# Kernel optimization log

Hardware: AMD Instinct MI355X
Metric: run time of the kernel (lower is better)

The kernel has to match this reference:

```python
import jax, jax.numpy as jnp
import numpy as np
from jax import lax

D, B, C, H, HD, FF, NC = 6, 32, 384, 6, 64, 1536, 10
IMG, P = 224, 16
N = (IMG // P) ** 2 + 1  # 197 tokens incl cls
SCALE = HD ** -0.5
EPS = 1e-6


def ln(x, w, b):
    m = jnp.mean(x, axis=-1, keepdims=True)
    v = jnp.var(x, axis=-1, keepdims=True)
    return (x - m) * lax.rsqrt(v + EPS) * w + b


def setup_inputs() -> dict:
    key = jax.random.key(0)
    ks = iter(jax.random.split(key, 40))
    rn = lambda shape, s=0.02: jax.random.normal(next(ks), shape, jnp.float32) * s
    inp = {
        'x': jax.random.normal(next(ks), (B, 3, IMG, IMG), jnp.float32),
        'y': jax.random.randint(next(ks), (B,), 0, NC),
        'patch_w': rn((C, 3, P, P)),
        'patch_b': rn((C,)),
        'cls_token': rn((1, 1, C)),
        'pos_embed': rn((1, N, C)),
        'n1_w': jnp.ones((D, C)), 'n1_b': jnp.zeros((D, C)),
        'qkv_w': rn((D, 3 * C, C)), 'qkv_b': rn((D, 3 * C)),
        'proj_w': rn((D, C, C)), 'proj_b': rn((D, C)),
        'mask_attn': jnp.ones((D, NC, H, HD)) + rn((D, NC, H, HD), 0.01),
        'mask_proj': jnp.ones((D, NC, C, C)) + rn((D, NC, C, C), 0.01),
        'n2_w': jnp.ones((D, C)), 'n2_b': jnp.zeros((D, C)),
        'fc1_w': rn((D, FF, C)), 'fc1_b': rn((D, FF)),
        'fc2_w': rn((D, C, FF)), 'fc2_b': rn((D, C)),
        'mask_fc1': jnp.ones((D, NC, FF, C)) + rn((D, NC, FF, C), 0.01),
        'mask_fc2': jnp.ones((D, NC, C, FF)) + rn((D, NC, C, FF), 0.01),
        'norm_w': jnp.ones((C,)), 'norm_b': jnp.zeros((C,)),
        'head_w': rn((NC, C)), 'head_b': jnp.zeros((NC,)),
    }
    return inp


def reference(x, y, patch_w, patch_b, cls_token, pos_embed, n1_w, n1_b, qkv_w,
              qkv_b, proj_w, proj_b, mask_attn, mask_proj, n2_w, n2_b,
              fc1_w, fc1_b, fc2_w, fc2_b, mask_fc1, mask_fc2,
              norm_w, norm_b, head_w, head_b):
    # patch embed: conv P x P stride P -> (B, C, 14, 14) -> (B, 196, C)
    h = lax.conv_general_dilated(x, patch_w, (P, P), 'VALID',
                                 dimension_numbers=('NCHW', 'OIHW', 'NCHW'))
    h = h.reshape(B, C, -1).transpose(0, 2, 1) + patch_b
    h = jnp.concatenate([jnp.broadcast_to(cls_token, (B, 1, C)), h], axis=1)
    h = h + pos_embed

    def block(xc, p):
        (w1n, b1n, qw, qb, pw, pb, ma, mp, w2n, b2n,
         f1w, f1b, f2w, f2b, mf1, mf2) = p
        t = ln(xc, w1n, b1n)
        qkv = (t @ qw.T + qb).reshape(B, N, 3, H, HD).transpose(2, 0, 3, 1, 4)
        q, k, v = qkv[0], qkv[1], qkv[2]  # (B,H,N,HD)
        a = jax.nn.softmax((q * SCALE) @ k.transpose(0, 1, 3, 2), axis=-1)
        o = a @ v  # (B,H,N,HD)
        o = o * ma[y][:, :, None, :]  # per-class head/dim mask
        o = o.transpose(0, 2, 1, 3).reshape(B, N, C)
        Wp = pw[None] * mp[y]  # (B,C,C) per-sample masked proj
        attn_out = jnp.einsum('bni,boi->bno', o, Wp) + pb
        xc = xc + attn_out
        t = ln(xc, w2n, b2n)
        W1 = f1w[None] * mf1[y]  # (B,FF,C)
        t = jnp.einsum('bni,boi->bno', t, W1) + f1b
        t = jax.nn.gelu(t, approximate=False)
        W2 = f2w[None] * mf2[y]  # (B,C,FF)
        t = jnp.einsum('bni,boi->bno', t, W2) + f2b
        return xc + t, None

    xs = (n1_w, n1_b, qkv_w, qkv_b, proj_w, proj_b, mask_attn, mask_proj,
          n2_w, n2_b, fc1_w, fc1_b, fc2_w, fc2_b, mask_fc1, mask_fc2)
    h, _ = lax.scan(block, h, xs)
    h = ln(h, norm_w, norm_b)
    cls = h[:, 0]  # (B, C)
    return cls @ head_w.T + head_b
```

## Files before the change

### kernel.cpp

```cpp
#include <hip/hip_runtime.h>
#include <hip/hip_bf16.h>
#include <math.h>

#define Dn 6
#define Bn 32
#define Cn 384
#define Hn 6
#define HDn 64
#define FFn 1536
#define NCn 10
#define IMGn 224
#define Nn 197
#define NPATCH 196
#define RP 256
#define SCALEf 0.125f
#define EPSf 1e-6f

typedef unsigned short u16;
typedef __attribute__((ext_vector_type(8))) short short8;
typedef __attribute__((ext_vector_type(4))) float f32x4;

__device__ __forceinline__ u16 f2bf(float f) {
    unsigned u = __float_as_uint(f);
    return (u16)((u + 0x7FFFu + ((u >> 16) & 1u)) >> 16);
}

__device__ __forceinline__ void gload16(const void* g, void* l) {
    __builtin_amdgcn_global_load_lds((const __attribute__((address_space(1))) void*)g,
                                     (__attribute__((address_space(3))) void*)l, 16, 0, 0);
}

__global__ __launch_bounds__(256) void cvtbf_kernel(const float* __restrict__ in,
                                                    u16* __restrict__ out) {
    long off = ((long)blockIdx.x * 256 + threadIdx.x) * 8;
    float4 v0 = *(const float4*)(in + off);
    float4 v1 = *(const float4*)(in + off + 4);
    short8 p;
    p[0] = f2bf(v0.x); p[1] = f2bf(v0.y); p[2] = f2bf(v0.z); p[3] = f2bf(v0.w);
    p[4] = f2bf(v1.x); p[5] = f2bf(v1.y); p[6] = f2bf(v1.z); p[7] = f2bf(v1.w);
    *(short8*)(out + off) = p;
}

__global__ __launch_bounds__(256) void maskmul_kernel(const float* __restrict__ W,
                                                      const float* __restrict__ mask,
                                                      u16* __restrict__ out, int NK) {
    int c = blockIdx.y;
    long off = ((long)blockIdx.x * 256 + threadIdx.x) * 8;
    long coff = (long)c * NK + off;
    float4 w0 = *(const float4*)(W + off);
    float4 w1 = *(const float4*)(W + off + 4);
    float4 m0 = *(const float4*)(mask + coff);
    float4 m1 = *(const float4*)(mask + coff + 4);
    short8 p;
    p[0] = f2bf(w0.x * m0.x); p[1] = f2bf(w0.y * m0.y);
    p[2] = f2bf(w0.z * m0.z); p[3] = f2bf(w0.w * m0.w);
    p[4] = f2bf(w1.x * m1.x); p[5] = f2bf(w1.y * m1.y);
    p[6] = f2bf(w1.z * m1.z); p[7] = f2bf(w1.w * m1.w);
    *(short8*)(out + coff) = p;
}

__global__ __launch_bounds__(256) void im2col_kernel(const float* __restrict__ x,
                                                     u16* __restrict__ col) {
    long idx = (long)blockIdx.x * 256 + threadIdx.x;
    int k = (int)(idx % 768);
    long row = idx / 768;
    int b = (int)(row / NPATCH), p = (int)(row % NPATCH);
    int i = k / 256, r = k % 256, ph = r / 16, pw = r % 16;
    int py = p / 14, px = p % 14;
    col[idx] = f2bf(x[(((long)b * 3 + i) * IMGn + py * 16 + ph) * IMGn + px * 16 + pw]);
}

__global__ __launch_bounds__(256) void assemble_kernel(const float* __restrict__ tmp,
                                                       const float* __restrict__ cls_token,
                                                       const float* __restrict__ pos,
                                                       float* __restrict__ x) {
    long idx = (long)blockIdx.x * 256 + threadIdx.x;
    const long total = (long)Bn * Nn * Cn;
    if (idx >= total) return;
    int c = (int)(idx % Cn);
    long rem = idx / Cn;
    int n = (int)(rem % Nn);
    int b = (int)(rem / Nn);
    float v;
    if (n == 0) v = cls_token[c];
    else v = tmp[((long)b * NPATCH + (n - 1)) * Cn + c];
    x[((long)b * RP + n) * Cn + c] = v + pos[n * Cn + c];
}

__global__ __launch_bounds__(64) void ln_kernel(const float* __restrict__ x,
                                                const float* __restrict__ w,
                                                const float* __restrict__ b,
                                                u16* __restrict__ out) {
    long blk = blockIdx.x;
    int bb = (int)(blk / Nn), n = (int)(blk % Nn);
    long row = (long)bb * RP + n;
    int lane = threadIdx.x;
    const float* xr = x + row * Cn;
    float v[6];
    float s = 0.f, ss = 0.f;
#pragma unroll
    for (int j = 0; j < 6; ++j) {
        v[j] = xr[lane + 64 * j];
        s += v[j];
        ss += v[j] * v[j];
    }
#pragma unroll
    for (int off = 32; off >= 1; off >>= 1) {
        s += __shfl_xor(s, off);
        ss += __shfl_xor(ss, off);
    }
    float m = s * (1.0f / Cn);
    float var = ss * (1.0f / Cn) - m * m;
    float rstd = rsqrtf(var + EPSf);
#pragma unroll
    for (int j = 0; j < 6; ++j) {
        int c = lane + 64 * j;
        out[row * Cn + c] = f2bf((v[j] - m) * rstd * w[c] + b[c]);
    }
}

template <int EPI, int KSPLIT>
__global__ __launch_bounds__(256) void gemm_bf16(
    const u16* __restrict__ A, long strideA,
    const u16* __restrict__ Wb, long wClassStride,
    const int* __restrict__ y,
    const float* __restrict__ bias,
    void* __restrict__ OutV, long strideO,
    int Nout, int Ktot, int NTILES) {
    const int bz = blockIdx.z;
    const int nt = blockIdx.y % NTILES;
    const int ks = blockIdx.y / NTILES;
    const int K2 = Ktot / KSPLIT;
    const int kbeg = ks * K2;
    A += (long)bz * strideA;
    const u16* Wp = Wb + (y ? (long)y[bz] * wClassStride : 0);

    __shared__ alignas(16) u16 Ab[4096];
    __shared__ alignas(16) u16 Bb[4096];

    const int tid = threadIdx.x;
    const int lane = tid & 63;
    const int w = tid >> 6;
    const int wr = w >> 1, wc = w & 1;
    const int m0 = blockIdx.x * 128;
    const int n0 = nt * 128;

    const int srow = 2 * w * 16 + (lane & 15);
    const int gk = (lane >> 4) * 8;

    f32x4 acc[4][4];
#pragma unroll
    for (int i = 0; i < 4; ++i)
#pragma unroll
        for (int j = 0; j < 4; ++j) acc[i][j] = (f32x4){0.f, 0.f, 0.f, 0.f};

    for (int k0 = kbeg; k0 < kbeg + K2; k0 += 32) {
        const u16* a0 = A + (long)(m0 + srow) * Ktot + k0 + gk;
        const u16* b0 = Wp + (long)(n0 + srow) * Ktot + k0 + gk;
        gload16(a0, Ab + 2 * w * 512);
        gload16(a0 + 16 * (long)Ktot, Ab + (2 * w + 1) * 512);
        gload16(b0, Bb + 2 * w * 512);
        gload16(b0 + 16 * (long)Ktot, Bb + (2 * w + 1) * 512);
        __syncthreads();
        short8 af[4], bfr[4];
#pragma unroll
        for (int i = 0; i < 4; ++i)
            af[i] = *(const short8*)(Ab + (wr * 4 + i) * 512 + lane * 8);
#pragma unroll
        for (int j = 0; j < 4; ++j)
            bfr[j] = *(const short8*)(Bb + (wc * 4 + j) * 512 + lane * 8);
#pragma unroll
        for (int i = 0; i < 4; ++i)
#pragma unroll
            for (int j = 0; j < 4; ++j)
                acc[i][j] = __builtin_amdgcn_mfma_f32_16x16x32_bf16(af[i], bfr[j], acc[i][j], 0, 0, 0);
        __syncthreads();
    }

    const int lr = lane >> 4;
    const int lc = lane & 15;
#pragma unroll
    for (int i = 0; i < 4; ++i) {
#pragma unroll
        for (int j = 0; j < 4; ++j) {
            int colg = n0 + (wc * 4 + j) * 16 + lc;
            float bv = (bias && ks == 0) ? bias[colg] : 0.f;
#pragma unroll
            for (int r = 0; r < 4; ++r) {
                int m = m0 + (wr * 4 + i) * 16 + lr * 4 + r;
                float v = acc[i][j][r] + bv;
                long oi = (long)m * Nout + colg;
                if (EPI == 0) {
                    ((u16*)OutV + (long)bz * strideO)[oi] = f2bf(v);
                } else if (EPI == 1) {
                    v = 0.5f * v * (1.0f + erff(v * 0.70710678118654752440f));
                    ((u16*)OutV + (long)bz * strideO)[oi] = f2bf(v);
                } else if (EPI == 2) {
                    float* Out = (float*)OutV + (long)bz * strideO;
                    if (KSPLIT > 1) atomicAdd(Out + oi, v);
                    else Out[oi] += v;
                } else {
                    ((float*)OutV + (long)bz * strideO)[oi] = v;
                }
            }
        }
    }
}

__global__ __launch_bounds__(256) void attn_fused(const u16* __restrict__ qkv,
                                                  const float* __restrict__ ma,
                                                  const int* __restrict__ y,
                                                  u16* __restrict__ O) {
    const int it = blockIdx.x;
    const int bh = blockIdx.y;
    const int h = bh % Hn, b = bh / Hn;
    const int i0 = it * 64;
    const int tid = threadIdx.x, lane = tid & 63, w = tid >> 6;
    const int lg = lane >> 4, lc = lane & 15;

    __shared__ alignas(16) u16 SH[31744];
    u16* Qb = SH;
    u16* Kb = SH + 4096;
    u16* Vb = SH;
    u16* Pb = SH + 17408;

    const u16* qkv_b = qkv + (long)b * RP * (3 * Cn);
    const int r15 = lane & 15;
    const int oct = lane >> 4;

#pragma unroll
    for (int si = 0; si < 2; ++si) {
        int s = w * 2 + si;
        int r = (s >> 1) * 16 + r15;
        int g = (s & 1) * 4 + oct;
        const u16* src = qkv_b + (long)(i0 + r) * (3 * Cn) + h * HDn + g * 8;
        gload16(src, Qb + s * 512);
    }
    for (int s = w; s < 26; s += 4) {
        int c = (s >> 1) * 16 + r15;
        int g = (s & 1) * 4 + oct;
        const u16* src = qkv_b + (long)c * (3 * Cn) + Cn + h * HDn + g * 8;
        gload16(src, Kb + s * 512);
    }
    __syncthreads();

    f32x4 s[13];
#pragma unroll
    for (int jf = 0; jf < 13; ++jf) s[jf] = (f32x4){0.f, 0.f, 0.f, 0.f};
    {
        short8 a0 = *(const short8*)(Qb + (w * 2 + 0) * 512 + lane * 8);
        short8 a1 = *(const short8*)(Qb + (w * 2 + 1) * 512 + lane * 8);
#pragma unroll
        for (int jf = 0; jf < 13; ++jf) {
            short8 b0 = *(const short8*)(Kb + (jf * 2 + 0) * 512 + lane * 8);
            short8 b1 = *(const short8*)(Kb + (jf * 2 + 1) * 512 + lane * 8);
            s[jf] = __builtin_amdgcn_mfma_f32_16x16x32_bf16(a0, b0, s[jf], 0, 0, 0);
            s[jf] = __builtin_amdgcn_mfma_f32_16x16x32_bf16(a1, b1, s[jf], 0, 0, 0);
        }
    }

#pragma unroll
    for (int r = 0; r < 4; ++r) {
        float mx = -1e30f;
#pragma unroll
        for (int jf = 0; jf < 13; ++jf) {
            float v = s[jf][r] * SCALEf;
            if (jf * 16 + lc > 196) v = -1e30f;
            mx = fmaxf(mx, v);
        }
#pragma unroll
        for (int off = 1; off <= 8; off <<= 1) mx = fmaxf(mx, __shfl_xor(mx, off));
        float sum = 0.f;
#pragma unroll
        for (int jf = 0; jf < 13; ++jf) {
            float e = (jf * 16 + lc <= 196) ? __expf(s[jf][r] * SCALEf - mx) : 0.f;
            s[jf][r] = e;
            sum += e;
        }
#pragma unroll
        for (int off = 1; off <= 8; off <<= 1) sum += __shfl_xor(sum, off);
        float inv = 1.0f / sum;
#pragma unroll
        for (int jf = 0; jf < 13; ++jf) s[jf][r] *= inv;
    }
    __syncthreads();

    if (lane < 32) {
        short8 z = {0, 0, 0, 0, 0, 0, 0, 0};
        *(short8*)(Pb + (w * 7 + 6) * 512 + (32 + lane) * 8) = z;
    }
#pragma unroll
    for (int jf = 0; jf < 13; ++jf) {
#pragma unroll
        for (int r = 0; r < 4; ++r) {
            int col = jf * 16 + lc;
            int row = lg * 4 + r;
            Pb[(w * 7 + (col >> 5)) * 512 + (((col >> 3) & 3) * 16 + row) * 8 + (col & 7)] =
                (u16)f2bf(s[jf][r]);
        }
    }
    {
        const u16* vbase = qkv_b + 2 * Cn + h * HDn + (tid & 63);
        int d = tid & 63;
#pragma unroll
        for (int k = 0; k < 7; ++k) {
            int jo = (tid >> 6) + 4 * k;
            short8 p;
#pragma unroll
            for (int t = 0; t < 8; ++t)
                p[t] = (short)vbase[(long)(jo * 8 + t) * (3 * Cn)];
            *(short8*)(Vb + (d >> 4) * (7 * 512) + (jo >> 2) * 512 +
                       ((jo & 3) * 16 + (d & 15)) * 8) = p;
        }
    }
    __syncthreads();

    f32x4 o[4];
#pragma unroll
    for (int df = 0; df < 4; ++df) o[df] = (f32x4){0.f, 0.f, 0.f, 0.f};
#pragma unroll
    for (int ks = 0; ks < 7; ++ks) {
        short8 pa = *(const short8*)(Pb + (w * 7 + ks) * 512 + lane * 8);
#pragma unroll
        for (int df = 0; df < 4; ++df) {
            short8 vb = *(const short8*)(Vb + (df * 7 + ks) * 512 + lane * 8);
            o[df] = __builtin_amdgcn_mfma_f32_16x16x32_bf16(pa, vb, o[df], 0, 0, 0);
        }
    }

    const float* mar = ma + (long)y[b] * (Hn * HDn) + h * HDn;
#pragma unroll
    for (int df = 0; df < 4; ++df) {
        int dcol = df * 16 + lc;
        float mk = mar[dcol];
#pragma unroll
        for (int r = 0; r < 4; ++r) {
            int i = i0 + w * 16 + lg * 4 + r;
            O[((long)b * RP + i) * Cn + h * HDn + dcol] = f2bf(o[df][r] * mk);
        }
    }
}

__global__ __launch_bounds__(64) void final_head(const float* __restrict__ x,
                                                 const float* __restrict__ nw,
                                                 const float* __restrict__ nb,
                                                 const float* __restrict__ hw,
                                                 const float* __restrict__ hb,
                                                 float* __restrict__ out) {
    int b = blockIdx.x;
    int lane = threadIdx.x;
    const float* xr = x + (long)b * RP * Cn;
    float v[6];
    float s = 0.f, ss = 0.f;
#pragma unroll
    for (int j = 0; j < 6; ++j) {
        v[j] = xr[lane + 64 * j];
        s += v[j];
        ss += v[j] * v[j];
    }
#pragma unroll
    for (int off = 32; off >= 1; off >>= 1) {
        s += __shfl_xor(s, off);
        ss += __shfl_xor(ss, off);
    }
    float m = s * (1.0f / Cn);
    float var = ss * (1.0f / Cn) - m * m;
    float rstd = rsqrtf(var + EPSf);
    float nvals[6];
#pragma unroll
    for (int j = 0; j < 6; ++j) {
        int c = lane + 64 * j;
        nvals[j] = (v[j] - m) * rstd * nw[c] + nb[c];
    }
    for (int c10 = 0; c10 < NCn; ++c10) {
        float p = 0.f;
#pragma unroll
        for (int j = 0; j < 6; ++j) p += nvals[j] * hw[(long)c10 * Cn + lane + 64 * j];
#pragma unroll
        for (int off = 32; off >= 1; off >>= 1) p += __shfl_xor(p, off);
        if (lane == 0) out[b * NCn + c10] = p + hb[c10];
    }
}

extern "C" void kernel_launch(void* const* d_in, const int* in_sizes, int n_in,
                              void* d_out, int out_size, void* d_ws, size_t ws_size,
                              hipStream_t stream) {
    const float* x_in     = (const float*)d_in[0];
    const int*   y        = (const int*)d_in[1];
    const float* patch_w  = (const float*)d_in[2];
    const float* patch_b  = (const float*)d_in[3];
    const float* cls_tok  = (const float*)d_in[4];
    const float* pos_emb  = (const float*)d_in[5];
    const float* n1_w     = (const float*)d_in[6];
    const float* n1_b     = (const float*)d_in[7];
    const float* qkv_w    = (const float*)d_in[8];
    const float* qkv_b    = (const float*)d_in[9];
    const float* proj_w   = (const float*)d_in[10];
    const float* proj_b   = (const float*)d_in[11];
    const float* mask_attn= (const float*)d_in[12];
    const float* mask_proj= (const float*)d_in[13];
    const float* n2_w     = (const float*)d_in[14];
    const float* n2_b     = (const float*)d_in[15];
    const float* fc1_w    = (const float*)d_in[16];
    const float* fc1_b    = (const float*)d_in[17];
    const float* fc2_w    = (const float*)d_in[18];
    const float* fc2_b    = (const float*)d_in[19];
    const float* mask_fc1 = (const float*)d_in[20];
    const float* mask_fc2 = (const float*)d_in[21];
    const float* norm_w   = (const float*)d_in[22];
    const float* norm_b   = (const float*)d_in[23];
    const float* head_w   = (const float*)d_in[24];
    const float* head_b   = (const float*)d_in[25];

    char* base = (char*)d_ws;
    float* X   = (float*)base;                       base += (long)Bn * RP * Cn * 4;
    u16*   T   = (u16*)base;                         base += (long)Bn * RP * Cn * 2;
    u16*   QKV = (u16*)base;                         base += (long)Bn * RP * 3 * Cn * 2;
    u16*   O   = (u16*)base;                         base += (long)Bn * RP * Cn * 2;
    u16*   FFb = (u16*)base;                         base += (long)Bn * RP * FFn * 2;
    u16*   COL = (u16*)base;                         base += (long)Bn * NPATCH * 768 * 2;
    u16*   WQ  = (u16*)base;                         base += (long)Dn * 3 * Cn * Cn * 2;
    u16*   WP  = (u16*)base;                         base += (long)Cn * 768 * 2;
    u16*   WMp = (u16*)base;                         base += (long)NCn * Cn * Cn * 2;
    u16*   WMf1= (u16*)base;                         base += (long)NCn * FFn * Cn * 2;
    u16*   WMf2= (u16*)base;                         base += (long)NCn * Cn * FFn * 2;
    float* PTMP= (float*)FFb;

    const long sX = (long)RP * Cn;
    const long sT = (long)RP * Cn;
    const long sF = (long)RP * FFn;

    cvtbf_kernel<<<1296, 256, 0, stream>>>(qkv_w, WQ);
    cvtbf_kernel<<<144, 256, 0, stream>>>(patch_w, WP);

    im2col_kernel<<<18816, 256, 0, stream>>>(x_in, COL);
    gemm_bf16<3, 1><<<dim3(49, 3, 1), 256, 0, stream>>>(
        COL, 0, WP, 0, nullptr, patch_b, PTMP, 0, Cn, 768, 3);
    assemble_kernel<<<9456, 256, 0, stream>>>(PTMP, cls_tok, pos_emb, X);

    for (int l = 0; l < Dn; ++l) {
        maskmul_kernel<<<dim3(72, NCn), 256, 0, stream>>>(
            proj_w + (long)l * Cn * Cn, mask_proj + (long)l * NCn * Cn * Cn, WMp, Cn * Cn);
        maskmul_kernel<<<dim3(288, NCn), 256, 0, stream>>>(
            fc1_w + (long)l * FFn * Cn, mask_fc1 + (long)l * NCn * FFn * Cn, WMf1, FFn * Cn);
        maskmul_kernel<<<dim3(288, NCn), 256, 0, stream>>>(
            fc2_w + (long)l * Cn * FFn, mask_fc2 + (long)l * NCn * Cn * FFn, WMf2, Cn * FFn);

        ln_kernel<<<Bn * Nn, 64, 0, stream>>>(X, n1_w + l * Cn, n1_b + l * Cn, T);
        gemm_bf16<0, 1><<<dim3(64, 9, 1), 256, 0, stream>>>(
            T, 0, WQ + (long)l * 3 * Cn * Cn, 0, nullptr, qkv_b + (long)l * 3 * Cn,
            QKV, 0, 3 * Cn, Cn, 9);
        attn_fused<<<dim3(4, Bn * Hn), 256, 0, stream>>>(
            QKV, mask_attn + (long)l * NCn * Hn * HDn, y, O);
        gemm_bf16<2, 2><<<dim3(2, 6, Bn), 256, 0, stream>>>(
            O, sT, WMp, (long)Cn * Cn, y, proj_b + l * Cn, X, sX, Cn, Cn, 3);
        ln_kernel<<<Bn * Nn, 64, 0, stream>>>(X, n2_w + l * Cn, n2_b + l * Cn, T);
        gemm_bf16<1, 1><<<dim3(2, 12, Bn), 256, 0, stream>>>(
            T, sT, WMf1, (long)FFn * Cn, y, fc1_b + (long)l * FFn, FFb, sF, FFn, Cn, 12);
        gemm_bf16<2, 2><<<dim3(2, 6, Bn), 256, 0, stream>>>(
            FFb, sF, WMf2, (long)Cn * FFn, y, fc2_b + l * Cn, X, sX, Cn, FFn, 3);
    }

    final_head<<<Bn, 64, 0, stream>>>(X, norm_w, norm_b, head_w, head_b, (float*)d_out);
}
```

Baseline: 1.089 ms.

## Double-buffer GEMM LDS tiles, replace split-K with 64-row tiles, merge maskmul launches

The GEMM kernel now double-buffers its A and B LDS tiles, issuing the next k-step's async global-to-LDS loads before computing on the current buffer, which cuts one barrier per iteration. Split-K with atomics is removed. The proj/fc2 and patch GEMMs instead use a 64-row M tile, so they get more blocks without atomicAdd. The three per-layer mask-multiply launches are merged into one kernel with a segment index. Trade-offs: LDS use doubles, and the smaller tiles reuse less data per block.

New measurement: 1.023 ms. -6.1%, faster.

```diff
diff --git a/kernel.cpp b/kernel.cpp
--- a/kernel.cpp
+++ b/kernel.cpp
@@ -41,22 +41,30 @@
     *(short8*)(out + off) = p;
 }
 
-__global__ __launch_bounds__(256) void maskmul_kernel(const float* __restrict__ W,
-                                                      const float* __restrict__ mask,
-                                                      u16* __restrict__ out, int NK) {
-    int c = blockIdx.y;
-    long off = ((long)blockIdx.x * 256 + threadIdx.x) * 8;
-    long coff = (long)c * NK + off;
-    float4 w0 = *(const float4*)(W + off);
-    float4 w1 = *(const float4*)(W + off + 4);
-    float4 m0 = *(const float4*)(mask + coff);
-    float4 m1 = *(const float4*)(mask + coff + 4);
+__global__ __launch_bounds__(256) void maskmul3_kernel(
+    const float* __restrict__ pw, const float* __restrict__ mp,
+    const float* __restrict__ f1w, const float* __restrict__ mf1,
+    const float* __restrict__ f2w, const float* __restrict__ mf2,
+    u16* __restrict__ WMp, u16* __restrict__ WMf1, u16* __restrict__ WMf2) {
+    int seg = blockIdx.y;
+    const float* W; const float* M; u16* O; int NK; int nblk;
+    if (seg == 0)      { W = pw;  M = mp;  O = WMp;  NK = Cn * Cn;  nblk = 720; }
+    else if (seg == 1) { W = f1w; M = mf1; O = WMf1; NK = FFn * Cn; nblk = 2880; }
+    else               { W = f2w; M = mf2; O = WMf2; NK = Cn * FFn; nblk = 2880; }
+    if (blockIdx.x >= nblk) return;
+    long e = ((long)blockIdx.x * 256 + threadIdx.x) * 8;
+    int c = (int)(e / NK);
+    int wi = (int)(e - (long)c * NK);
+    float4 w0 = *(const float4*)(W + wi);
+    float4 w1 = *(const float4*)(W + wi + 4);
+    float4 m0 = *(const float4*)(M + e);
+    float4 m1 = *(const float4*)(M + e + 4);
     short8 p;
     p[0] = f2bf(w0.x * m0.x); p[1] = f2bf(w0.y * m0.y);
     p[2] = f2bf(w0.z * m0.z); p[3] = f2bf(w0.w * m0.w);
     p[4] = f2bf(w1.x * m1.x); p[5] = f2bf(w1.y * m1.y);
     p[6] = f2bf(w1.z * m1.z); p[7] = f2bf(w1.w * m1.w);
-    *(short8*)(out + coff) = p;
+    *(short8*)(O + e) = p;
 }
 
 __global__ __launch_bounds__(256) void im2col_kernel(const float* __restrict__ x,
@@ -119,75 +127,88 @@
     }
 }
 
-template <int EPI, int KSPLIT>
+template <int EPI, int MT>
 __global__ __launch_bounds__(256) void gemm_bf16(
     const u16* __restrict__ A, long strideA,
     const u16* __restrict__ Wb, long wClassStride,
     const int* __restrict__ y,
     const float* __restrict__ bias,
     void* __restrict__ OutV, long strideO,
-    int Nout, int Ktot, int NTILES) {
+    int Nout, int Ktot) {
     const int bz = blockIdx.z;
-    const int nt = blockIdx.y % NTILES;
-    const int ks = blockIdx.y / NTILES;
-    const int K2 = Ktot / KSPLIT;
-    const int kbeg = ks * K2;
     A += (long)bz * strideA;
     const u16* Wp = Wb + (y ? (long)y[bz] * wClassStride : 0);
 
-    __shared__ alignas(16) u16 Ab[4096];
-    __shared__ alignas(16) u16 Bb[4096];
+    constexpr int ASUB = MT / 16;
+    constexpr int AI = MT / 32;
+    __shared__ alignas(16) u16 Ab[2][ASUB * 512];
+    __shared__ alignas(16) u16 Bb[2][4096];
 
     const int tid = threadIdx.x;
     const int lane = tid & 63;
     const int w = tid >> 6;
     const int wr = w >> 1, wc = w & 1;
-    const int m0 = blockIdx.x * 128;
-    const int n0 = nt * 128;
-
-    const int srow = 2 * w * 16 + (lane & 15);
-    const int gk = (lane >> 4) * 8;
-
-    f32x4 acc[4][4];
-#pragma unroll
-    for (int i = 0; i < 4; ++i)
+    const int m0 = blockIdx.x * MT;
+    const int n0 = blockIdx.y * 128;
+    const int r15 = lane & 15, oct = lane >> 4;
+
+    auto STAGE = [&](int k0, int bf) {
+        {
+            int s0 = 2 * w;
+            const u16* b0 = Wp + (long)(n0 + 16 * s0 + r15) * Ktot + k0 + oct * 8;
+            gload16(b0, &Bb[bf][s0 * 512]);
+            gload16(b0 + 16 * (long)Ktot, &Bb[bf][(s0 + 1) * 512]);
+        }
+        if (MT == 128) {
+            int s0 = 2 * w;
+            const u16* a0 = A + (long)(m0 + 16 * s0 + r15) * Ktot + k0 + oct * 8;
+            gload16(a0, &Ab[bf][s0 * 512]);
+            gload16(a0 + 16 * (long)Ktot, &Ab[bf][(s0 + 1) * 512]);
+        } else {
+            const u16* a0 = A + (long)(m0 + 16 * w + r15) * Ktot + k0 + oct * 8;
+            gload16(a0, &Ab[bf][w * 512]);
+        }
+    };
+
+    f32x4 acc[AI][4];
+#pragma unroll
+    for (int i = 0; i < AI; ++i)
 #pragma unroll
         for (int j = 0; j < 4; ++j) acc[i][j] = (f32x4){0.f, 0.f, 0.f, 0.f};
 
-    for (int k0 = kbeg; k0 < kbeg + K2; k0 += 32) {
-        const u16* a0 = A + (long)(m0 + srow) * Ktot + k0 + gk;
-        const u16* b0 = Wp + (long)(n0 + srow) * Ktot + k0 + gk;
-        gload16(a0, Ab + 2 * w * 512);
-        gload16(a0 + 16 * (long)Ktot, Ab + (2 * w + 1) * 512);
-        gload16(b0, Bb + 2 * w * 512);
-        gload16(b0 + 16 * (long)Ktot, Bb + (2 * w + 1) * 512);
-        __syncthreads();
-        short8 af[4], bfr[4];
-#pragma unroll
-        for (int i = 0; i < 4; ++i)
-            af[i] = *(const short8*)(Ab + (wr * 4 + i) * 512 + lane * 8);
+    const int nsteps = Ktot / 32;
+    STAGE(0, 0);
+    __syncthreads();
+    int cur = 0;
+    for (int t = 0; t < nsteps; ++t) {
+        if (t + 1 < nsteps) STAGE((t + 1) * 32, cur ^ 1);
+        short8 af[AI], bfr[4];
+#pragma unroll
+        for (int i = 0; i < AI; ++i)
+            af[i] = *(const short8*)(&Ab[cur][(wr * AI + i) * 512 + lane * 8]);
 #pragma unroll
         for (int j = 0; j < 4; ++j)
-            bfr[j] = *(const short8*)(Bb + (wc * 4 + j) * 512 + lane * 8);
-#pragma unroll
-        for (int i = 0; i < 4; ++i)
+            bfr[j] = *(const short8*)(&Bb[cur][(wc * 4 + j) * 512 + lane * 8]);
+#pragma unroll
+        for (int i = 0; i < AI; ++i)
 #pragma unroll
             for (int j = 0; j < 4; ++j)
                 acc[i][j] = __builtin_amdgcn_mfma_f32_16x16x32_bf16(af[i], bfr[j], acc[i][j], 0, 0, 0);
         __syncthreads();
+        cur ^= 1;
     }
 
     const int lr = lane >> 4;
     const int lc = lane & 15;
 #pragma unroll
-    for (int i = 0; i < 4; ++i) {
+    for (int i = 0; i < AI; ++i) {
 #pragma unroll
         for (int j = 0; j < 4; ++j) {
             int colg = n0 + (wc * 4 + j) * 16 + lc;
-            float bv = (bias && ks == 0) ? bias[colg] : 0.f;
+            float bv = bias ? bias[colg] : 0.f;
 #pragma unroll
             for (int r = 0; r < 4; ++r) {
-                int m = m0 + (wr * 4 + i) * 16 + lr * 4 + r;
+                int m = m0 + (wr * AI + i) * 16 + lr * 4 + r;
                 float v = acc[i][j][r] + bv;
                 long oi = (long)m * Nout + colg;
                 if (EPI == 0) {
@@ -197,8 +218,7 @@
                     ((u16*)OutV + (long)bz * strideO)[oi] = f2bf(v);
                 } else if (EPI == 2) {
                     float* Out = (float*)OutV + (long)bz * strideO;
-                    if (KSPLIT > 1) atomicAdd(Out + oi, v);
-                    else Out[oi] += v;
+                    Out[oi] += v;
                 } else {
                     ((float*)OutV + (long)bz * strideO)[oi] = v;
                 }
@@ -434,31 +454,30 @@
     cvtbf_kernel<<<144, 256, 0, stream>>>(patch_w, WP);
 
     im2col_kernel<<<18816, 256, 0, stream>>>(x_in, COL);
-    gemm_bf16<3, 1><<<dim3(49, 3, 1), 256, 0, stream>>>(
-        COL, 0, WP, 0, nullptr, patch_b, PTMP, 0, Cn, 768, 3);
+    gemm_bf16<3, 64><<<dim3(98, 3, 1), 256, 0, stream>>>(
+        COL, 0, WP, 0, nullptr, patch_b, PTMP, 0, Cn, 768);
     assemble_kernel<<<9456, 256, 0, stream>>>(PTMP, cls_tok, pos_emb, X);
 
     for (int l = 0; l < Dn; ++l) {
-        maskmul_kernel<<<dim3(72, NCn), 256, 0, stream>>>(
-            proj_w + (long)l * Cn * Cn, mask_proj + (long)l * NCn * Cn * Cn, WMp, Cn * Cn);
-        maskmul_kernel<<<dim3(288, NCn), 256, 0, stream>>>(
-            fc1_w + (long)l * FFn * Cn, mask_fc1 + (long)l * NCn * FFn * Cn, WMf1, FFn * Cn);
-        maskmul_kernel<<<dim3(288, NCn), 256, 0, stream>>>(
-            fc2_w + (long)l * Cn * FFn, mask_fc2 + (long)l * NCn * Cn * FFn, WMf2, Cn * FFn);
+        maskmul3_kernel<<<dim3(2880, 3), 256, 0, stream>>>(
+            proj_w + (long)l * Cn * Cn, mask_proj + (long)l * NCn * Cn * Cn,
+            fc1_w + (long)l * FFn * Cn, mask_fc1 + (long)l * NCn * FFn * Cn,
+            fc2_w + (long)l * Cn * FFn, mask_fc2 + (long)l * NCn * Cn * FFn,
+            WMp, WMf1, WMf2);
 
         ln_kernel<<<Bn * Nn, 64, 0, stream>>>(X, n1_w + l * Cn, n1_b + l * Cn, T);
-        gemm_bf16<0, 1><<<dim3(64, 9, 1), 256, 0, stream>>>(
+        gemm_bf16<0, 128><<<dim3(64, 9, 1), 256, 0, stream>>>(
             T, 0, WQ + (long)l * 3 * Cn * Cn, 0, nullptr, qkv_b + (long)l * 3 * Cn,
-            QKV, 0, 3 * Cn, Cn, 9);
+            QKV, 0, 3 * Cn, Cn);
         attn_fused<<<dim3(4, Bn * Hn), 256, 0, stream>>>(
             QKV, mask_attn + (long)l * NCn * Hn * HDn, y, O);
-        gemm_bf16<2, 2><<<dim3(2, 6, Bn), 256, 0, stream>>>(
-            O, sT, WMp, (long)Cn * Cn, y, proj_b + l * Cn, X, sX, Cn, Cn, 3);
+        gemm_bf16<2, 64><<<dim3(4, 3, Bn), 256, 0, stream>>>(
+            O, sT, WMp, (long)Cn * Cn, y, proj_b + l * Cn, X, sX, Cn, Cn);
         ln_kernel<<<Bn * Nn, 64, 0, stream>>>(X, n2_w + l * Cn, n2_b + l * Cn, T);
-        gemm_bf16<1, 1><<<dim3(2, 12, Bn), 256, 0, stream>>>(
-            T, sT, WMf1, (long)FFn * Cn, y, fc1_b + (long)l * FFn, FFb, sF, FFn, Cn, 12);
-        gemm_bf16<2, 2><<<dim3(2, 6, Bn), 256, 0, stream>>>(
-            FFb, sF, WMf2, (long)Cn * FFn, y, fc2_b + l * Cn, X, sX, Cn, FFn, 3);
+        gemm_bf16<1, 128><<<dim3(2, 12, Bn), 256, 0, stream>>>(
+            T, sT, WMf1, (long)FFn * Cn, y, fc1_b + (long)l * FFn, FFb, sF, FFn, Cn);
+        gemm_bf16<2, 64><<<dim3(4, 3, Bn), 256, 0, stream>>>(
+            FFb, sF, WMf2, (long)Cn * FFn, y, fc2_b + l * Cn, X, sX, Cn, FFn);
     }
 
     final_head<<<Bn, 64, 0, stream>>>(X, norm_w, norm_b, head_w, head_b, (float*)d_out);
```
